# Kernel tuning notes

Measured on AMD Instinct MI355X. Metric: run time of the kernel, lower is better.

Reference implementation:

```python
import jax, jax.numpy as jnp
import numpy as np
import math

B, S, D, H = 2, 2048, 1024, 16
DK = D // H


def setup_inputs() -> dict:
    key = jax.random.key(0)
    ks = jax.random.split(key, 12)
    scale = 1.0 / math.sqrt(D)
    inp = {
        "query": jax.random.normal(ks[0], (B, S, D), jnp.float32),
        "key": jax.random.normal(ks[1], (B, S, D), jnp.float32),
        "value": jax.random.normal(ks[2], (B, S, D), jnp.float32),
        # causal 0/1 mask, broadcast over heads
        "mask": jnp.broadcast_to(jnp.tril(jnp.ones((S, S), jnp.int32)), (B, 1, S, S)),
        "Wq": jax.random.normal(ks[3], (D, D), jnp.float32) * scale,
        "bq": jnp.zeros((D,), jnp.float32),
        "Wk": jax.random.normal(ks[4], (D, D), jnp.float32) * scale,
        "bk": jnp.zeros((D,), jnp.float32),
        "Wv": jax.random.normal(ks[5], (D, D), jnp.float32) * scale,
        "bv": jnp.zeros((D,), jnp.float32),
        "Wo": jax.random.normal(ks[6], (D, D), jnp.float32) * scale,
        "bo": jnp.zeros((D,), jnp.float32),
    }
    return inp


def _split_heads(x):
    # [B,S,D] -> [B,H,S,DK]
    return x.reshape(B, S, H, DK).transpose(0, 2, 1, 3)


def reference(query, key, value, mask, Wq, bq, Wk, bk, Wv, bv, Wo, bo):
    q = _split_heads(query @ Wq.T + bq)
    k = _split_heads(key @ Wk.T + bk)
    v = _split_heads(value @ Wv.T + bv)
    # scaled dot-product attention with additive mask (mask==0 -> -inf)
    scores = jnp.einsum("bhqd,bhkd->bhqk", q, k) / math.sqrt(DK)
    scores = jnp.where(mask == 0, -jnp.inf, scores)
    w = jax.nn.softmax(scores, axis=-1)
    out = jnp.einsum("bhqk,bhkd->bhqd", w, v)
    out = out.transpose(0, 2, 1, 3).reshape(B, S, D)
    return out @ Wo.T + bo
```

## Files before the change

### kernel.cpp

```cpp
#include <hip/hip_runtime.h>
#include <hip/hip_bf16.h>
#include <math.h>

#define BBATCH 2
#define SSEQ 2048
#define DMODEL 1024
#define NH 16
#define MTOT (BBATCH*SSEQ)

typedef short bfrag __attribute__((ext_vector_type(8)));
typedef float ffrag __attribute__((ext_vector_type(4)));

typedef const __attribute__((address_space(1))) unsigned int* gas_t;
typedef __attribute__((address_space(3))) unsigned int* las_t;

__device__ __forceinline__ void dl16(const void* g, void* l) {
  __builtin_amdgcn_global_load_lds((gas_t)(unsigned long long)g,
                                   (las_t)(unsigned int)(unsigned long long)l,
                                   16, 0, 0);
}

__device__ __forceinline__ unsigned short f2bf(float f) {
  union { float f; unsigned u; } v; v.f = f;
  unsigned r = v.u + 0x7fffu + ((v.u >> 16) & 1u);
  return (unsigned short)(r >> 16);
}

__global__ __launch_bounds__(256) void convert_all_kernel(
    const float* __restrict__ q, const float* __restrict__ k, const float* __restrict__ v,
    const float* __restrict__ wq, const float* __restrict__ wk,
    const float* __restrict__ wv, const float* __restrict__ wo,
    unsigned short* __restrict__ dst)
{
  const long NIN = (long)MTOT * DMODEL;
  const long NW  = (long)DMODEL * DMODEL;
  const long total4 = (3 * NIN + 4 * NW) >> 2;
  long i4 = (long)blockIdx.x * blockDim.x + threadIdx.x;
  const long stride = (long)gridDim.x * blockDim.x;
  for (; i4 < total4; i4 += stride) {
    const long i = i4 << 2;
    const float* src; long off;
    if (i < NIN)          { src = q; off = i; }
    else if (i < 2 * NIN) { src = k; off = i - NIN; }
    else if (i < 3 * NIN) { src = v; off = i - 2 * NIN; }
    else {
      const long j = i - 3 * NIN;
      const int wsel = (int)(j >> 20);
      off = j & (NW - 1);
      src = (wsel == 0) ? wq : (wsel == 1) ? wk : (wsel == 2) ? wv : wo;
    }
    const float4 x = *(const float4*)(src + off);
    ushort4 o;
    o.x = f2bf(x.x); o.y = f2bf(x.y); o.z = f2bf(x.z); o.w = f2bf(x.w);
    *(ushort4*)(dst + i) = o;
  }
}

struct ProjArgs {
  const unsigned short* X[3];
  const unsigned short* W[3];
  const float* bias[3];
  unsigned short* dst[3];
  float scale[3];
};

__global__ __launch_bounds__(256, 2) void qkv_proj(ProjArgs a)
{
  __shared__ alignas(16) unsigned short As[128 * 64];
  __shared__ alignas(16) unsigned short Bs[64 * 64];
  const int t = threadIdx.x;
  const int lane = t & 63, w = t >> 6;
  const int quad = lane >> 4, l16 = lane & 15;
  const int m0 = blockIdx.x * 128;
  const int n0 = blockIdx.y * 64;
  const int z = blockIdx.z;
  const unsigned short* __restrict__ X = a.X[z];
  const unsigned short* __restrict__ W = a.W[z];
  const int wm = (w & 1) * 64, wn = (w >> 1) * 32;

  ffrag acc[4][2];
#pragma unroll
  for (int i = 0; i < 4; ++i)
#pragma unroll
    for (int j = 0; j < 2; ++j)
#pragma unroll
      for (int e = 0; e < 4; ++e) acc[i][j][e] = 0.f;

  for (int kk = 0; kk < 16; ++kk) {
    const int k0 = kk * 64;
    __syncthreads();
#pragma unroll
    for (int i = 0; i < 4; ++i) {
      const int ch = i * 256 + t;
      dl16(X + (size_t)(m0 + (ch >> 3)) * DMODEL + k0 + (ch & 7) * 8, As + ch * 8);
    }
#pragma unroll
    for (int i = 0; i < 2; ++i) {
      const int ch = i * 256 + t;
      dl16(W + (size_t)(n0 + (ch >> 3)) * DMODEL + k0 + (ch & 7) * 8, Bs + ch * 8);
    }
    __syncthreads();

    bfrag af[4][2], bg[2][2];
#pragma unroll
    for (int fi = 0; fi < 4; ++fi)
#pragma unroll
      for (int c = 0; c < 2; ++c)
        af[fi][c] = *(const bfrag*)&As[(wm + fi * 16 + l16) * 64 + c * 32 + quad * 8];
#pragma unroll
    for (int fj = 0; fj < 2; ++fj)
#pragma unroll
      for (int c = 0; c < 2; ++c)
        bg[fj][c] = *(const bfrag*)&Bs[(wn + fj * 16 + l16) * 64 + c * 32 + quad * 8];
#pragma unroll
    for (int c = 0; c < 2; ++c)
#pragma unroll
      for (int fi = 0; fi < 4; ++fi)
#pragma unroll
        for (int fj = 0; fj < 2; ++fj)
          acc[fi][fj] = __builtin_amdgcn_mfma_f32_16x16x32_bf16(af[fi][c], bg[fj][c], acc[fi][fj], 0, 0, 0);
  }

  const float sc = a.scale[z];
  const float* __restrict__ bias = a.bias[z];
  unsigned short* __restrict__ dst = a.dst[z];
#pragma unroll
  for (int fj = 0; fj < 2; ++fj) {
    const int n = n0 + wn + fj * 16 + l16;
    const float bv = bias[n];
    const int h = n >> 6, dk = n & 63;
    if (z < 2) {
#pragma unroll
      for (int fi = 0; fi < 4; ++fi)
#pragma unroll
        for (int r = 0; r < 4; ++r) {
          const int m = m0 + wm + fi * 16 + quad * 4 + r;
          const int b_ = m >> 11, s_ = m & (SSEQ - 1);
          dst[((size_t)(b_ * NH + h) * SSEQ + s_) * 64 + dk] = f2bf((acc[fi][fj][r] + bv) * sc);
        }
    } else {
#pragma unroll
      for (int fi = 0; fi < 4; ++fi) {
        const int m = m0 + wm + fi * 16 + quad * 4;
        const int b_ = m >> 11, s_ = m & (SSEQ - 1);
        ushort4 pk;
        pk.x = f2bf(acc[fi][fj][0] + bv);
        pk.y = f2bf(acc[fi][fj][1] + bv);
        pk.z = f2bf(acc[fi][fj][2] + bv);
        pk.w = f2bf(acc[fi][fj][3] + bv);
        *(ushort4*)&dst[((size_t)(b_ * NH + h) * 64 + dk) * SSEQ + s_] = pk;
      }
    }
  }
}

__global__ __launch_bounds__(256, 2) void out_proj(
    const unsigned short* __restrict__ X,
    const unsigned short* __restrict__ W,
    const float* __restrict__ bias,
    float* __restrict__ Y)
{
  __shared__ alignas(16) unsigned short As[128 * 64];
  __shared__ alignas(16) unsigned short Bs[64 * 64];
  const int t = threadIdx.x;
  const int lane = t & 63, w = t >> 6;
  const int quad = lane >> 4, l16 = lane & 15;
  const int m0 = blockIdx.x * 128;
  const int n0 = blockIdx.y * 64;
  const int wm = (w & 1) * 64, wn = (w >> 1) * 32;

  ffrag acc[4][2];
#pragma unroll
  for (int i = 0; i < 4; ++i)
#pragma unroll
    for (int j = 0; j < 2; ++j)
#pragma unroll
      for (int e = 0; e < 4; ++e) acc[i][j][e] = 0.f;

  for (int kk = 0; kk < 16; ++kk) {
    const int k0 = kk * 64;
    __syncthreads();
#pragma unroll
    for (int i = 0; i < 4; ++i) {
      const int ch = i * 256 + t;
      dl16(X + (size_t)(m0 + (ch >> 3)) * DMODEL + k0 + (ch & 7) * 8, As + ch * 8);
    }
#pragma unroll
    for (int i = 0; i < 2; ++i) {
      const int ch = i * 256 + t;
      dl16(W + (size_t)(n0 + (ch >> 3)) * DMODEL + k0 + (ch & 7) * 8, Bs + ch * 8);
    }
    __syncthreads();

    bfrag af[4][2], bg[2][2];
#pragma unroll
    for (int fi = 0; fi < 4; ++fi)
#pragma unroll
      for (int c = 0; c < 2; ++c)
        af[fi][c] = *(const bfrag*)&As[(wm + fi * 16 + l16) * 64 + c * 32 + quad * 8];
#pragma unroll
    for (int fj = 0; fj < 2; ++fj)
#pragma unroll
      for (int c = 0; c < 2; ++c)
        bg[fj][c] = *(const bfrag*)&Bs[(wn + fj * 16 + l16) * 64 + c * 32 + quad * 8];
#pragma unroll
    for (int c = 0; c < 2; ++c)
#pragma unroll
      for (int fi = 0; fi < 4; ++fi)
#pragma unroll
        for (int fj = 0; fj < 2; ++fj)
          acc[fi][fj] = __builtin_amdgcn_mfma_f32_16x16x32_bf16(af[fi][c], bg[fj][c], acc[fi][fj], 0, 0, 0);
  }

#pragma unroll
  for (int fj = 0; fj < 2; ++fj) {
    const int n = n0 + wn + fj * 16 + l16;
    const float bv = bias[n];
#pragma unroll
    for (int fi = 0; fi < 4; ++fi)
#pragma unroll
      for (int r = 0; r < 4; ++r) {
        const int m = m0 + wm + fi * 16 + quad * 4 + r;
        Y[(size_t)m * DMODEL + n] = acc[fi][fj][r] + bv;
      }
  }
}

__global__ __launch_bounds__(256, 4) void attn_mfma(
    const unsigned short* __restrict__ Q,
    const unsigned short* __restrict__ K,
    const unsigned short* __restrict__ Vt_g,
    unsigned short* __restrict__ ctx)
{
  __shared__ alignas(16) unsigned short Kt[64 * 64];
  __shared__ alignas(16) unsigned short Vt[64 * 64];
  __shared__ alignas(16) unsigned short Pt[4][16 * 72];

  const int t = threadIdx.x;
  const int lane = t & 63, w = t >> 6;
  const int quad = lane >> 4, l16 = lane & 15;
  const int bh = blockIdx.y;
  const int qtile = blockIdx.z ? (31 - (int)blockIdx.x) : (int)blockIdx.x;
  const int i0 = qtile * 64;
  const int b_ = bh >> 4, h_ = bh & (NH - 1);
  const int q_l = w * 16 + l16;

  const unsigned short* qg = Q + ((size_t)bh * SSEQ + i0) * 64;
  bfrag qb[2];
#pragma unroll
  for (int c = 0; c < 2; ++c)
    qb[c] = *(const bfrag*)(qg + (size_t)q_l * 64 + c * 32 + quad * 8);

  ffrag o[4];
#pragma unroll
  for (int fn = 0; fn < 4; ++fn)
#pragma unroll
    for (int e = 0; e < 4; ++e) o[fn][e] = 0.f;
  float lsum = 0.f;

  const unsigned short* kg = K + (size_t)bh * SSEQ * 64;
  const unsigned short* vg = Vt_g + (size_t)bh * 64 * SSEQ;

  for (int jt = 0; jt <= qtile; ++jt) {
    __syncthreads();
#pragma unroll
    for (int i = 0; i < 2; ++i) {
      const int ch = i * 256 + t;
      dl16(kg + (size_t)(jt * 64) * 64 + ch * 8, Kt + ch * 8);
      dl16(vg + (size_t)(ch >> 3) * SSEQ + jt * 64 + (ch & 7) * 8, Vt + ch * 8);
    }
    __syncthreads();

    ffrag s[4];
#pragma unroll
    for (int fj = 0; fj < 4; ++fj)
#pragma unroll
      for (int e = 0; e < 4; ++e) s[fj][e] = 0.f;
#pragma unroll
    for (int c = 0; c < 2; ++c)
#pragma unroll
      for (int fj = 0; fj < 4; ++fj) {
        bfrag ka = *(const bfrag*)&Kt[(fj * 16 + l16) * 64 + c * 32 + quad * 8];
        s[fj] = __builtin_amdgcn_mfma_f32_16x16x32_bf16(ka, qb[c], s[fj], 0, 0, 0);
      }

    const bool diag = (jt == qtile);
#pragma unroll
    for (int fj = 0; fj < 4; ++fj) {
      float p[4];
#pragma unroll
      for (int r = 0; r < 4; ++r) {
        float pe = exp2f(s[fj][r]);
        if (diag && (fj * 16 + quad * 4 + r) > q_l) pe = 0.f;
        p[r] = pe;
        lsum += pe;
      }
      float2 lo; lo.x = p[0]; lo.y = p[1];
      float2 hi; hi.x = p[2]; hi.y = p[3];
      union { __hip_bfloat162 h[2]; unsigned long long u; } cv;
      cv.h[0] = __float22bfloat162_rn(lo);
      cv.h[1] = __float22bfloat162_rn(hi);
      *(unsigned long long*)&Pt[w][l16 * 72 + fj * 16 + quad * 4] = cv.u;
    }
    asm volatile("s_waitcnt lgkmcnt(0)" ::: "memory");

#pragma unroll
    for (int c = 0; c < 2; ++c) {
      bfrag pb = *(const bfrag*)&Pt[w][l16 * 72 + c * 32 + quad * 8];
#pragma unroll
      for (int fn = 0; fn < 4; ++fn) {
        bfrag va = *(const bfrag*)&Vt[(fn * 16 + l16) * 64 + c * 32 + quad * 8];
        o[fn] = __builtin_amdgcn_mfma_f32_16x16x32_bf16(va, pb, o[fn], 0, 0, 0);
      }
    }
  }

  lsum += __shfl_xor(lsum, 16);
  lsum += __shfl_xor(lsum, 32);

  const float inv = 1.f / lsum;
  unsigned short* cbase = ctx + (size_t)(b_ * SSEQ + i0 + q_l) * DMODEL + h_ * 64;
#pragma unroll
  for (int fn = 0; fn < 4; ++fn) {
    float2 lo; lo.x = o[fn][0] * inv; lo.y = o[fn][1] * inv;
    float2 hi; hi.x = o[fn][2] * inv; hi.y = o[fn][3] * inv;
    union { __hip_bfloat162 h[2]; unsigned long long u; } cv;
    cv.h[0] = __float22bfloat162_rn(lo);
    cv.h[1] = __float22bfloat162_rn(hi);
    *(unsigned long long*)(cbase + fn * 16 + quad * 4) = cv.u;
  }
}

extern "C" void kernel_launch(void* const* d_in, const int* in_sizes, int n_in,
                              void* d_out, int out_size, void* d_ws, size_t ws_size,
                              hipStream_t stream)
{
  const float* q  = (const float*)d_in[0];
  const float* k  = (const float*)d_in[1];
  const float* v  = (const float*)d_in[2];
  const float* wq = (const float*)d_in[4];
  const float* bq = (const float*)d_in[5];
  const float* wk = (const float*)d_in[6];
  const float* bk = (const float*)d_in[7];
  const float* wv = (const float*)d_in[8];
  const float* bv = (const float*)d_in[9];
  const float* wo = (const float*)d_in[10];
  const float* bo = (const float*)d_in[11];

  const long NIN = (long)MTOT * DMODEL;
  const long NW  = (long)DMODEL * DMODEL;
  unsigned short* ws16 = (unsigned short*)d_ws;
  unsigned short* qx  = ws16;
  unsigned short* kx  = qx + NIN;
  unsigned short* vx  = kx + NIN;
  unsigned short* wqb = vx + NIN;
  unsigned short* wkb = wqb + NW;
  unsigned short* wvb = wkb + NW;
  unsigned short* wob = wvb + NW;
  unsigned short* Qp  = wob + NW;
  unsigned short* Kp  = Qp + NIN;
  unsigned short* Vp  = Kp + NIN;
  unsigned short* Cx  = Vp + NIN;

  convert_all_kernel<<<2048, 256, 0, stream>>>(q, k, v, wq, wk, wv, wo, ws16);

  ProjArgs pa;
  pa.X[0] = qx;  pa.X[1] = kx;  pa.X[2] = vx;
  pa.W[0] = wqb; pa.W[1] = wkb; pa.W[2] = wvb;
  pa.bias[0] = bq; pa.bias[1] = bk; pa.bias[2] = bv;
  pa.dst[0] = Qp; pa.dst[1] = Kp; pa.dst[2] = Vp;
  pa.scale[0] = 0.18033688011112042f;
  pa.scale[1] = 1.0f;
  pa.scale[2] = 1.0f;
  qkv_proj<<<dim3(MTOT / 128, DMODEL / 64, 3), 256, 0, stream>>>(pa);

  attn_mfma<<<dim3(16, BBATCH * NH, 2), 256, 0, stream>>>(Qp, Kp, Vp, Cx);

  out_proj<<<dim3(MTOT / 128, DMODEL / 64), 256, 0, stream>>>(Cx, wob, bo, (float*)d_out);
}
```

Baseline: 251.6 us.

## Double-buffer K/V tiles with swizzled LDS in attention; enlarge GEMM tiles

```diff
diff --git a/kernel.cpp b/kernel.cpp
--- a/kernel.cpp
+++ b/kernel.cpp
@@ -18,6 +18,10 @@
   __builtin_amdgcn_global_load_lds((gas_t)(unsigned long long)g,
                                    (las_t)(unsigned int)(unsigned long long)l,
                                    16, 0, 0);
+}
+
+__device__ __forceinline__ void drain_vm() {
+  asm volatile("s_waitcnt vmcnt(0)" ::: "memory");
 }
 
 __device__ __forceinline__ unsigned short f2bf(float f) {
@@ -67,22 +71,22 @@
 __global__ __launch_bounds__(256, 2) void qkv_proj(ProjArgs a)
 {
   __shared__ alignas(16) unsigned short As[128 * 64];
-  __shared__ alignas(16) unsigned short Bs[64 * 64];
+  __shared__ alignas(16) unsigned short Bs[128 * 64];
   const int t = threadIdx.x;
   const int lane = t & 63, w = t >> 6;
   const int quad = lane >> 4, l16 = lane & 15;
   const int m0 = blockIdx.x * 128;
-  const int n0 = blockIdx.y * 64;
+  const int n0 = blockIdx.y * 128;
   const int z = blockIdx.z;
   const unsigned short* __restrict__ X = a.X[z];
   const unsigned short* __restrict__ W = a.W[z];
-  const int wm = (w & 1) * 64, wn = (w >> 1) * 32;
-
-  ffrag acc[4][2];
+  const int wm = (w & 1) * 64, wn = (w >> 1) * 64;
+
+  ffrag acc[4][4];
 #pragma unroll
   for (int i = 0; i < 4; ++i)
 #pragma unroll
-    for (int j = 0; j < 2; ++j)
+    for (int j = 0; j < 4; ++j)
 #pragma unroll
       for (int e = 0; e < 4; ++e) acc[i][j][e] = 0.f;
 
@@ -92,32 +96,27 @@
 #pragma unroll
     for (int i = 0; i < 4; ++i) {
       const int ch = i * 256 + t;
-      dl16(X + (size_t)(m0 + (ch >> 3)) * DMODEL + k0 + (ch & 7) * 8, As + ch * 8);
-    }
-#pragma unroll
-    for (int i = 0; i < 2; ++i) {
-      const int ch = i * 256 + t;
-      dl16(W + (size_t)(n0 + (ch >> 3)) * DMODEL + k0 + (ch & 7) * 8, Bs + ch * 8);
-    }
+      const int row = ch >> 3, pc = ch & 7;
+      dl16(X + (size_t)(m0 + row) * DMODEL + k0 + pc * 8, As + ch * 8);
+      dl16(W + (size_t)(n0 + row) * DMODEL + k0 + pc * 8, Bs + ch * 8);
+    }
+    drain_vm();
     __syncthreads();
 
-    bfrag af[4][2], bg[2][2];
+    bfrag af[4][2], bg[4][2];
 #pragma unroll
     for (int fi = 0; fi < 4; ++fi)
 #pragma unroll
-      for (int c = 0; c < 2; ++c)
+      for (int c = 0; c < 2; ++c) {
         af[fi][c] = *(const bfrag*)&As[(wm + fi * 16 + l16) * 64 + c * 32 + quad * 8];
-#pragma unroll
-    for (int fj = 0; fj < 2; ++fj)
-#pragma unroll
-      for (int c = 0; c < 2; ++c)
-        bg[fj][c] = *(const bfrag*)&Bs[(wn + fj * 16 + l16) * 64 + c * 32 + quad * 8];
+        bg[fi][c] = *(const bfrag*)&Bs[(wn + fi * 16 + l16) * 64 + c * 32 + quad * 8];
+      }
 #pragma unroll
     for (int c = 0; c < 2; ++c)
 #pragma unroll
       for (int fi = 0; fi < 4; ++fi)
 #pragma unroll
-        for (int fj = 0; fj < 2; ++fj)
+        for (int fj = 0; fj < 4; ++fj)
           acc[fi][fj] = __builtin_amdgcn_mfma_f32_16x16x32_bf16(af[fi][c], bg[fj][c], acc[fi][fj], 0, 0, 0);
   }
 
@@ -125,7 +124,7 @@
   const float* __restrict__ bias = a.bias[z];
   unsigned short* __restrict__ dst = a.dst[z];
 #pragma unroll
-  for (int fj = 0; fj < 2; ++fj) {
+  for (int fj = 0; fj < 4; ++fj) {
     const int n = n0 + wn + fj * 16 + l16;
     const float bv = bias[n];
     const int h = n >> 6, dk = n & 63;
@@ -161,19 +160,19 @@
     float* __restrict__ Y)
 {
   __shared__ alignas(16) unsigned short As[128 * 64];
-  __shared__ alignas(16) unsigned short Bs[64 * 64];
+  __shared__ alignas(16) unsigned short Bs[128 * 64];
   const int t = threadIdx.x;
   const int lane = t & 63, w = t >> 6;
   const int quad = lane >> 4, l16 = lane & 15;
   const int m0 = blockIdx.x * 128;
-  const int n0 = blockIdx.y * 64;
-  const int wm = (w & 1) * 64, wn = (w >> 1) * 32;
-
-  ffrag acc[4][2];
+  const int n0 = blockIdx.y * 128;
+  const int wm = (w & 1) * 64, wn = (w >> 1) * 64;
+
+  ffrag acc[4][4];
 #pragma unroll
   for (int i = 0; i < 4; ++i)
 #pragma unroll
-    for (int j = 0; j < 2; ++j)
+    for (int j = 0; j < 4; ++j)
 #pragma unroll
       for (int e = 0; e < 4; ++e) acc[i][j][e] = 0.f;
 
@@ -183,37 +182,32 @@
 #pragma unroll
     for (int i = 0; i < 4; ++i) {
       const int ch = i * 256 + t;
-      dl16(X + (size_t)(m0 + (ch >> 3)) * DMODEL + k0 + (ch & 7) * 8, As + ch * 8);
-    }
-#pragma unroll
-    for (int i = 0; i < 2; ++i) {
-      const int ch = i * 256 + t;
-      dl16(W + (size_t)(n0 + (ch >> 3)) * DMODEL + k0 + (ch & 7) * 8, Bs + ch * 8);
-    }
+      const int row = ch >> 3, pc = ch & 7;
+      dl16(X + (size_t)(m0 + row) * DMODEL + k0 + pc * 8, As + ch * 8);
+      dl16(W + (size_t)(n0 + row) * DMODEL + k0 + pc * 8, Bs + ch * 8);
+    }
+    drain_vm();
     __syncthreads();
 
-    bfrag af[4][2], bg[2][2];
+    bfrag af[4][2], bg[4][2];
 #pragma unroll
     for (int fi = 0; fi < 4; ++fi)
 #pragma unroll
-      for (int c = 0; c < 2; ++c)
+      for (int c = 0; c < 2; ++c) {
         af[fi][c] = *(const bfrag*)&As[(wm + fi * 16 + l16) * 64 + c * 32 + quad * 8];
-#pragma unroll
-    for (int fj = 0; fj < 2; ++fj)
-#pragma unroll
-      for (int c = 0; c < 2; ++c)
-        bg[fj][c] = *(const bfrag*)&Bs[(wn + fj * 16 + l16) * 64 + c * 32 + quad * 8];
+        bg[fi][c] = *(const bfrag*)&Bs[(wn + fi * 16 + l16) * 64 + c * 32 + quad * 8];
+      }
 #pragma unroll
     for (int c = 0; c < 2; ++c)
 #pragma unroll
       for (int fi = 0; fi < 4; ++fi)
 #pragma unroll
-        for (int fj = 0; fj < 2; ++fj)
+        for (int fj = 0; fj < 4; ++fj)
           acc[fi][fj] = __builtin_amdgcn_mfma_f32_16x16x32_bf16(af[fi][c], bg[fj][c], acc[fi][fj], 0, 0, 0);
   }
 
 #pragma unroll
-  for (int fj = 0; fj < 2; ++fj) {
+  for (int fj = 0; fj < 4; ++fj) {
     const int n = n0 + wn + fj * 16 + l16;
     const float bv = bias[n];
 #pragma unroll
@@ -232,9 +226,9 @@
     const unsigned short* __restrict__ Vt_g,
     unsigned short* __restrict__ ctx)
 {
-  __shared__ alignas(16) unsigned short Kt[64 * 64];
-  __shared__ alignas(16) unsigned short Vt[64 * 64];
-  __shared__ alignas(16) unsigned short Pt[4][16 * 72];
+  __shared__ alignas(16) unsigned short Kb[2][64 * 64];
+  __shared__ alignas(16) unsigned short Vb[2][64 * 64];
+  __shared__ alignas(16) unsigned short Pt[4][16 * 64];
 
   const int t = threadIdx.x;
   const int lane = t & 63, w = t >> 6;
@@ -245,7 +239,32 @@
   const int b_ = bh >> 4, h_ = bh & (NH - 1);
   const int q_l = w * 16 + l16;
 
+  const unsigned short* kg = K + (size_t)bh * SSEQ * 64;
+  const unsigned short* vg = Vt_g + (size_t)bh * 64 * SSEQ;
+
+  int koff[2], voff[2], loff[2];
+#pragma unroll
+  for (int i = 0; i < 2; ++i) {
+    const int ch = i * 256 + t;
+    const int r = ch >> 3;
+    const int lc = (ch & 7) ^ (r & 7);
+    koff[i] = r * 64 + lc * 8;
+    voff[i] = r * SSEQ + lc * 8;
+    loff[i] = ch * 8;
+  }
+  int sw[2];
+#pragma unroll
+  for (int c = 0; c < 2; ++c) sw[c] = (((c * 4 + quad) ^ (l16 & 7)) * 8);
+  const int pwr = l16 * 64 + (quad & 1) * 4;
+
   const unsigned short* qg = Q + ((size_t)bh * SSEQ + i0) * 64;
+
+#pragma unroll
+  for (int i = 0; i < 2; ++i) {
+    dl16(kg + koff[i], Kb[0] + loff[i]);
+    dl16(vg + voff[i], Vb[0] + loff[i]);
+  }
+
   bfrag qb[2];
 #pragma unroll
   for (int c = 0; c < 2; ++c)
@@ -258,18 +277,19 @@
     for (int e = 0; e < 4; ++e) o[fn][e] = 0.f;
   float lsum = 0.f;
 
-  const unsigned short* kg = K + (size_t)bh * SSEQ * 64;
-  const unsigned short* vg = Vt_g + (size_t)bh * 64 * SSEQ;
-
   for (int jt = 0; jt <= qtile; ++jt) {
+    const int cur = jt & 1;
+    drain_vm();
     __syncthreads();
-#pragma unroll
-    for (int i = 0; i < 2; ++i) {
-      const int ch = i * 256 + t;
-      dl16(kg + (size_t)(jt * 64) * 64 + ch * 8, Kt + ch * 8);
-      dl16(vg + (size_t)(ch >> 3) * SSEQ + jt * 64 + (ch & 7) * 8, Vt + ch * 8);
-    }
-    __syncthreads();
+
+    if (jt < qtile) {
+      const int nxt = cur ^ 1;
+#pragma unroll
+      for (int i = 0; i < 2; ++i) {
+        dl16(kg + (size_t)(jt + 1) * 4096 + koff[i], Kb[nxt] + loff[i]);
+        dl16(vg + (size_t)(jt + 1) * 64   + voff[i], Vb[nxt] + loff[i]);
+      }
+    }
 
     ffrag s[4];
 #pragma unroll
@@ -280,7 +300,7 @@
     for (int c = 0; c < 2; ++c)
 #pragma unroll
       for (int fj = 0; fj < 4; ++fj) {
-        bfrag ka = *(const bfrag*)&Kt[(fj * 16 + l16) * 64 + c * 32 + quad * 8];
+        bfrag ka = *(const bfrag*)&Kb[cur][(fj * 16 + l16) * 64 + sw[c]];
         s[fj] = __builtin_amdgcn_mfma_f32_16x16x32_bf16(ka, qb[c], s[fj], 0, 0, 0);
       }
 
@@ -300,16 +320,17 @@
       union { __hip_bfloat162 h[2]; unsigned long long u; } cv;
       cv.h[0] = __float22bfloat162_rn(lo);
       cv.h[1] = __float22bfloat162_rn(hi);
-      *(unsigned long long*)&Pt[w][l16 * 72 + fj * 16 + quad * 4] = cv.u;
+      const int cc = fj * 2 + (quad >> 1);
+      *(unsigned long long*)&Pt[w][pwr + ((cc ^ (l16 & 7)) * 8)] = cv.u;
     }
     asm volatile("s_waitcnt lgkmcnt(0)" ::: "memory");
 
 #pragma unroll
     for (int c = 0; c < 2; ++c) {
-      bfrag pb = *(const bfrag*)&Pt[w][l16 * 72 + c * 32 + quad * 8];
+      bfrag pb = *(const bfrag*)&Pt[w][l16 * 64 + sw[c]];
 #pragma unroll
       for (int fn = 0; fn < 4; ++fn) {
-        bfrag va = *(const bfrag*)&Vt[(fn * 16 + l16) * 64 + c * 32 + quad * 8];
+        bfrag va = *(const bfrag*)&Vb[cur][(fn * 16 + l16) * 64 + sw[c]];
         o[fn] = __builtin_amdgcn_mfma_f32_16x16x32_bf16(va, pb, o[fn], 0, 0, 0);
       }
     }
@@ -372,9 +393,9 @@
   pa.scale[0] = 0.18033688011112042f;
   pa.scale[1] = 1.0f;
   pa.scale[2] = 1.0f;
-  qkv_proj<<<dim3(MTOT / 128, DMODEL / 64, 3), 256, 0, stream>>>(pa);
+  qkv_proj<<<dim3(MTOT / 128, DMODEL / 128, 3), 256, 0, stream>>>(pa);
 
   attn_mfma<<<dim3(16, BBATCH * NH, 2), 256, 0, stream>>>(Qp, Kp, Vp, Cx);
 
-  out_proj<<<dim3(MTOT / 128, DMODEL / 64), 256, 0, stream>>>(Cx, wob, bo, (float*)d_out);
-}
+  out_proj<<<dim3(MTOT / 128, DMODEL / 128), 256, 0, stream>>>(Cx, wob, bo, (float*)d_out);
+}
```

Result: faster. 238.4 us (-5.2%).
